# Kernel optimization log

Measured on AMD Instinct MI355X. Metric: run time of the kernel, lower is better.

Reference implementation:

```python
import jax, jax.numpy as jnp
import numpy as np

L = 8       # num decoder layers
S = 192     # seq_len = h*w = 24*8
D = 512     # d_model
DFF = 2048  # dim_feedforward
H, W, BS = 24, 8, 16
EPS = 1e-5


def setup_inputs() -> dict:
    key = jax.random.key(0)
    ks = jax.random.split(key, 8)
    f = jax.random.normal
    return {
        "q_feat": f(ks[0], (BS, D * L, H, W), jnp.float32),
        "g_feat": f(ks[1], (BS, D * L, H, W), jnp.float32),
        "targets": jax.random.randint(ks[2], (BS,), 0, 8),
        "score_embed": f(ks[3], (L, S, S), jnp.float32) * 0.05,
        "fc0_w": f(ks[4], (L, D, D), jnp.float32) * (1.0 / np.sqrt(D)),
        "fc0_b": jnp.zeros((L, D), jnp.float32),
        "bn1_g": jnp.ones((L,), jnp.float32),
        "bn1_b": jnp.zeros((L,), jnp.float32),
        "fc2_w": f(ks[5], (L, DFF, S), jnp.float32) * (1.0 / np.sqrt(S)),
        "fc2_b": jnp.zeros((L, DFF), jnp.float32),
        "bn2_g": jnp.ones((L, DFF), jnp.float32),
        "bn2_b": jnp.zeros((L, DFF), jnp.float32),
        "fc3_w": f(ks[6], (L, DFF), jnp.float32) * (1.0 / np.sqrt(DFF)),
        "fc3_b": jnp.zeros((L,), jnp.float32),
        "bn3_g": jnp.ones((L,), jnp.float32),
        "bn3_b": jnp.zeros((L,), jnp.float32),
    }


def _layer(qf, gf, se, w0, b0, g1, b1, w2, b2, g2, bb2, w3, b3, g3, bb3):
    # qf: [q,s,d], gf: [k,s,d]; shared fc0 projection for query and key
    query = jnp.einsum('qsd,ed->qse', qf, w0) + b0
    key_ = jnp.einsum('ksd,ed->kse', gf, w0) + b0
    # 4D correlation volume masked by sigmoid of learned score embedding
    score = jnp.einsum('qtd,ksd->qkst', query, key_) * jax.nn.sigmoid(se)
    q, k = score.shape[0], score.shape[1]
    sc = score.reshape(q * k, S, S)
    cat = jnp.concatenate([sc.max(axis=1), sc.max(axis=2)], axis=-1)  # [qk, 2S]
    x = cat.reshape(-1, S)  # [2qk, S]  (matches torch view(-1,1,S))
    # bn1: single channel -> normalize over all elements (training-mode BN)
    x = g1 * (x - x.mean()) * jax.lax.rsqrt(x.var() + EPS) + b1
    x = x @ w2.T + b2  # [2qk, DFF]
    mu = x.mean(0)
    var = x.var(0)
    x = g2 * (x - mu) * jax.lax.rsqrt(var + EPS) + bb2
    x = jax.nn.relu(x)
    x = x @ w3 + b3  # [2qk]
    x = x.reshape(-1, 2).sum(-1)  # [qk]: sum of row-max branch and col-max branch
    x = g3 * (x - x.mean()) * jax.lax.rsqrt(x.var() + EPS) + bb3
    return x.reshape(q, k)


def reference(q_feat, g_feat, targets, score_embed, fc0_w, fc0_b, bn1_g, bn1_b,
              fc2_w, fc2_b, bn2_g, bn2_b, fc3_w, fc3_b, bn3_g, bn3_b):
    bs = q_feat.shape[0]
    qf = jnp.transpose(q_feat, (0, 2, 3, 1)).reshape(bs, S, D * L)
    gf = jnp.transpose(g_feat, (0, 2, 3, 1)).reshape(bs, S, D * L)
    score = None
    for i in range(L):  # fixed small layer loop; each layer has distinct params
        si = _layer(qf[..., i * D:(i + 1) * D], gf[..., i * D:(i + 1) * D],
                    score_embed[i], fc0_w[i], fc0_b[i], bn1_g[i], bn1_b[i],
                    fc2_w[i], fc2_b[i], bn2_g[i], bn2_b[i],
                    fc3_w[i], fc3_b[i], bn3_g[i], bn3_b[i])
        score = si if score is None else score + si
    pair_labels = (targets[:, None] == targets[None, :]).astype(jnp.float32)
    return score, pair_labels
```

## Files before the change

kernel.cpp:

```cpp
#include <hip/hip_runtime.h>
#include <hip/hip_bf16.h>


#define EPS_ 1e-5f

typedef __attribute__((ext_vector_type(8))) _Float16 fp16x8;
typedef __attribute__((ext_vector_type(4)))  float   f32x4;
typedef __attribute__((ext_vector_type(16))) float   f32x16;

__device__ __forceinline__ unsigned fkey(float f) {
    unsigned u = __float_as_uint(f);
    return (u & 0x80000000u) ? ~u : (u | 0x80000000u);
}
__device__ __forceinline__ float funkey(unsigned k) {
    return (k & 0x80000000u) ? __uint_as_float(k & 0x7FFFFFFFu)
                             : __uint_as_float(~k);
}
__device__ __forceinline__ void gld16(const void* gp, void* lp) {
    __builtin_amdgcn_global_load_lds(
        (const __attribute__((address_space(1))) unsigned*)gp,
        (__attribute__((address_space(3))) unsigned*)lp, 16, 0, 0);
}

__global__ __launch_bounds__(256) void k_prep(const float* __restrict__ se,
                                              float* __restrict__ sig,
                                              const float* __restrict__ w2,
                                              _Float16* __restrict__ w2h,
                                              unsigned* __restrict__ xkey,
                                              float* __restrict__ bn2z,
                                              const float* __restrict__ w0,
                                              _Float16* __restrict__ w0h) {
    int b = blockIdx.x;
    int tid = threadIdx.x;
    if (b < 3072) {
        int i = b * 256 + tid;
        float4 v = *(const float4*)(w2 + (size_t)i * 4);
        _Float16 h[4] = {(_Float16)v.x, (_Float16)v.y, (_Float16)v.z, (_Float16)v.w};
        *(uint2*)(w2h + (size_t)i * 4) = *(uint2*)h;
    } else if (b < 3360) {
        int i = (b - 3072) * 256 + tid;
        float4 v = *(const float4*)(se + (size_t)i * 4);
        float4 o;
        o.x = 1.f / (1.f + __expf(-v.x));
        o.y = 1.f / (1.f + __expf(-v.y));
        o.z = 1.f / (1.f + __expf(-v.z));
        o.w = 1.f / (1.f + __expf(-v.w));
        *(float4*)(sig + (size_t)i * 4) = o;
    } else if (b < 3552) {
        int i = (b - 3360) * 256 + tid;
        uint4 z = {0u, 0u, 0u, 0u};
        uint4* p = (uint4*)xkey + (size_t)i * 4;
        p[0] = z; p[1] = z; p[2] = z; p[3] = z;
    } else if (b < 3585) {
        int i = (b - 3552) * 256 + tid;
        if (i < 8196) {
            float4 z = {0.f, 0.f, 0.f, 0.f};
            *(float4*)(bn2z + (size_t)i * 4) = z;
        }
    } else {
        int g = (b - 3585) * 256 + tid;
        int l  = g >> 15;
        int r  = g & 32767;
        int ks = r >> 12;
        int rr = r & 4095;
        int e  = rr >> 3;
        int ch = rr & 7;
        const float* src = w0 + (size_t)l * 262144 + (size_t)e * 512 + ks * 64 + ch * 8;
        float4 v0 = *(const float4*)src;
        float4 v1 = *(const float4*)(src + 4);
        fp16x8 h;
        h[0] = (_Float16)v0.x; h[1] = (_Float16)v0.y; h[2] = (_Float16)v0.z; h[3] = (_Float16)v0.w;
        h[4] = (_Float16)v1.x; h[5] = (_Float16)v1.y; h[6] = (_Float16)v1.z; h[7] = (_Float16)v1.w;
        size_t dst = ((size_t)(l * 8 + ks) * 512 + e) * 8 + (ch ^ (e & 7));
        *(fp16x8*)(w0h + dst * 8) = h;
    }
}

__global__ __launch_bounds__(512, 4) void k_fc0(const float* __restrict__ qfeat,
                                                const float* __restrict__ gfeat,
                                                const _Float16* __restrict__ w0h,
                                                const float* __restrict__ b0,
                                                _Float16* __restrict__ Qh) {
    int bid = blockIdx.x;
    int blo = bid & 7;
    int et  = (bid >> 3) & 3;
    int bhi = (bid >> 5) & 1;
    int sel = (bid >> 6) & 1;
    int l   = bid >> 7;
    int b   = blo + bhi * 8;

    const float* feat = sel ? gfeat : qfeat;
    const float* Af = feat + (size_t)b * 786432 + (size_t)l * 98304;

    __shared__ __align__(16) char smem[81920];

    int tid = threadIdx.x;
    int lane = tid & 63;
    int w = tid >> 6;
    int wm = w >> 2, wn = w & 3;
    int c = lane & 15;
    int hi4 = lane >> 4;

    int s0 = tid, s1 = tid + 512, s2 = tid + 1024;
    int ch0 = s0 / 192, t0 = s0 - ch0 * 192;
    int ch1 = s1 / 192, t1 = s1 - ch1 * 192;
    int ch2 = s2 / 192, t2 = s2 - ch2 * 192;
    const float* ap0 = Af + ch0 * 1536 + t0;
    const float* ap1 = Af + ch1 * 1536 + t1;
    const float* ap2 = Af + ch2 * 1536 + t2;
    int aw0 = t0 * 128 + ((ch0 ^ (t0 & 7)) << 4);
    int aw1 = t1 * 128 + ((ch1 ^ (t1 & 7)) << 4);
    int aw2 = t2 * 128 + ((ch2 ^ (t2 & 7)) << 4);

    f32x4 acc[6][2];
    #pragma unroll
    for (int mi = 0; mi < 6; mi++)
        #pragma unroll
        for (int nj = 0; nj < 2; nj++)
            #pragma unroll
            for (int r = 0; r < 4; r++) acc[mi][nj][r] = 0.f;

    float rA[3][8];

    auto ALOAD = [&](int ks) {
        int off = ks * 12288;
        #pragma unroll
        for (int j = 0; j < 8; j++) rA[0][j] = ap0[off + j * 192];
        #pragma unroll
        for (int j = 0; j < 8; j++) rA[1][j] = ap1[off + j * 192];
        #pragma unroll
        for (int j = 0; j < 8; j++) rA[2][j] = ap2[off + j * 192];
    };
    auto WLOAD = [&](int ks, int buf) {
        const _Float16* wp = w0h + ((size_t)(l * 8 + ks) * 512 + et * 128) * 64;
        char* d = smem + 49152 + buf * 16384;
        #pragma unroll
        for (int p = 0; p < 2; p++)
            gld16(wp + (size_t)(tid + p * 512) * 8, d + (tid + p * 512) * 16);
    };
    auto AWRITE = [&](int buf) {
        char* db = smem + buf * 24576;
        fp16x8 h0, h1, h2;
        #pragma unroll
        for (int j = 0; j < 8; j++) h0[j] = (_Float16)rA[0][j];
        #pragma unroll
        for (int j = 0; j < 8; j++) h1[j] = (_Float16)rA[1][j];
        #pragma unroll
        for (int j = 0; j < 8; j++) h2[j] = (_Float16)rA[2][j];
        *(fp16x8*)(db + aw0) = h0;
        *(fp16x8*)(db + aw1) = h1;
        *(fp16x8*)(db + aw2) = h2;
    };
    auto COMPUTE = [&](int buf) {
        const char* Ab = smem + buf * 24576;
        const char* Wb = smem + 49152 + buf * 16384;
        fp16x8 afr[6][2], bfr[2][2];
        #pragma unroll
        for (int mi = 0; mi < 6; mi++) {
            int tr = wm * 96 + mi * 16 + c;
            #pragma unroll
            for (int k2 = 0; k2 < 2; k2++) {
                int ph = (k2 * 4 + hi4) ^ (tr & 7);
                afr[mi][k2] = *(const fp16x8*)(Ab + tr * 128 + ph * 16);
            }
        }
        #pragma unroll
        for (int nj = 0; nj < 2; nj++) {
            int er = wn * 32 + nj * 16 + c;
            #pragma unroll
            for (int k2 = 0; k2 < 2; k2++) {
                int ph = (k2 * 4 + hi4) ^ (er & 7);
                bfr[nj][k2] = *(const fp16x8*)(Wb + er * 128 + ph * 16);
            }
        }
        #pragma unroll
        for (int k2 = 0; k2 < 2; k2++)
            #pragma unroll
            for (int mi = 0; mi < 6; mi++)
                #pragma unroll
                for (int nj = 0; nj < 2; nj++)
                    acc[mi][nj] = __builtin_amdgcn_mfma_f32_16x16x32_f16(
                        afr[mi][k2], bfr[nj][k2], acc[mi][nj], 0, 0, 0);
    };

    ALOAD(0); WLOAD(0, 0); AWRITE(0);
    __syncthreads();
    #pragma unroll
    for (int ks = 0; ks < 8; ks++) {
        int cur = ks & 1, nxt = cur ^ 1;
        if (ks < 7) { ALOAD(ks + 1); WLOAD(ks + 1, nxt); }
        COMPUTE(cur);
        if (ks < 7) AWRITE(nxt);
        __syncthreads();
    }

    __syncthreads();
    _Float16* lb = (_Float16*)smem;
    int rq = hi4 * 4;
    #pragma unroll
    for (int nj = 0; nj < 2; nj++) {
        int col = wn * 32 + nj * 16 + c;
        float bias = b0[l * 512 + et * 128 + col];
        #pragma unroll
        for (int mi = 0; mi < 6; mi++) {
            int tb = wm * 96 + mi * 16 + rq;
            #pragma unroll
            for (int r = 0; r < 4; r++)
                lb[(tb + r) * 128 + col] = (_Float16)(acc[mi][nj][r] + bias);
        }
    }
    __syncthreads();
    _Float16* Ob = Qh + ((size_t)(sel * 8 + l) * 16 + b) * 98304 + et * 128;
    #pragma unroll
    for (int p = 0; p < 6; p++) {
        int v = tid + p * 512;
        int t = v >> 4;
        int e = (v & 15) * 8;
        *(fp16x8*)(Ob + (size_t)t * 512 + e) = *(const fp16x8*)(lb + t * 128 + e);
    }
}

#define BARP() do { __builtin_amdgcn_s_barrier(); \
                    __builtin_amdgcn_sched_barrier(0); } while (0)

__global__ __launch_bounds__(512, 2) void k_score(const _Float16* __restrict__ Qh,
                                                  const float* __restrict__ sig,
                                                  unsigned* __restrict__ xkey,
                                                  int base) {
    int bid = blockIdx.x + base;
    int l = bid & 7;
    int tau = bid >> 3;
    int mt = tau % 12;
    int nt = tau / 12;
    int m0 = mt * 256, n0 = nt * 256;

    const char* Ag = (const char*)(Qh + (size_t)(8 + l) * 1572864);
    const char* Bg = (const char*)(Qh + (size_t)l * 1572864);

    __shared__ __align__(16) char smem[131072];

    int tid = threadIdx.x;
    int lane = tid & 63;
    int w = tid >> 6;
    int wm = w >> 2, wn = w & 3;
    int c = lane & 15;
    int hi4 = lane >> 4;

    int pk0 = ((hi4)     ^ (c & 7)) * 16;
    int pk1 = ((4 + hi4) ^ (c & 7)) * 16;
    char* aBase = smem + wm * 16384 + c * 128;
    char* bBase = smem + 65536 + (wn >> 1) * 16384 + ((wn & 1) * 64 + c) * 128;

    int rl = lane >> 3;
    int qsw = ((lane & 7) ^ rl) * 16;
    const char* Asrc = Ag + (size_t)(m0 + w * 8 + rl) * 1024 + qsw;
    const char* Bsrc = Bg + (size_t)(n0 + w * 8 + rl) * 1024 + qsw;
    char* aSt = smem + w * 1024;
    char* bSt = smem + 65536 + w * 1024;

    f32x4 acc[8][4];
    #pragma unroll
    for (int mi = 0; mi < 8; mi++)
        #pragma unroll
        for (int nj = 0; nj < 4; nj++)
            #pragma unroll
            for (int r = 0; r < 4; r++) acc[mi][nj][r] = 0.f;

    fp16x8 a[4][2], b01[2][2], b23[2][2];

    auto STA = [&](int t, int h) {
        if (t < 8) {
            const char* s = Asrc + (size_t)(h * 128) * 1024 + t * 128;
            char* d = aSt + (t & 1) * 32768 + h * 16384;
            gld16(s, d);
            gld16(s + 64 * 1024, d + 8192);
        }
    };
    auto STB = [&](int t, int h) {
        if (t < 8) {
            const char* s = Bsrc + (size_t)(h * 128) * 1024 + t * 128;
            char* d = bSt + (t & 1) * 32768 + h * 16384;
            gld16(s, d);
            gld16(s + 64 * 1024, d + 8192);
        }
    };
    auto LDA = [&](int t, int mh) {
        const char* p = aBase + (t & 1) * 32768 + mh * 8192;
        #pragma unroll
        for (int m = 0; m < 4; m++) {
            a[m][0] = *(const fp16x8*)(p + m * 2048 + pk0);
            a[m][1] = *(const fp16x8*)(p + m * 2048 + pk1);
        }
    };
    auto LDB = [&](int t, int nh, fp16x8 (&bb)[2][2]) {
        const char* p = bBase + (t & 1) * 32768 + nh * 4096;
        #pragma unroll
        for (int n = 0; n < 2; n++) {
            bb[n][0] = *(const fp16x8*)(p + n * 2048 + pk0);
            bb[n][1] = *(const fp16x8*)(p + n * 2048 + pk1);
        }
    };
    auto MM = [&](int mh, int nh, fp16x8 (&bb)[2][2]) {
        #pragma unroll
        for (int ks = 0; ks < 2; ks++)
            #pragma unroll
            for (int m = 0; m < 4; m++)
                #pragma unroll
                for (int n = 0; n < 2; n++)
                    acc[mh * 4 + m][nh * 2 + n] = __builtin_amdgcn_mfma_f32_16x16x32_f16(
                        a[m][ks], bb[n][ks], acc[mh * 4 + m][nh * 2 + n], 0, 0, 0);
    };

    STB(0, 0); STB(0, 1); STA(0, 0); STA(0, 1); STB(1, 0); STB(1, 1);
    asm volatile("s_waitcnt vmcnt(4)");
    BARP();

    #pragma unroll
    for (int it = 0; it < 4; it++) {
        int T = 2 * it, U = 2 * it + 1;
        LDA(T, 0); LDB(T, 0, b01); STA(U, 0); BARP();
        __builtin_amdgcn_s_setprio(1); MM(0, 0, b01); __builtin_amdgcn_s_setprio(0); BARP();
        LDB(T, 1, b23); STA(U, 1); BARP();
        __builtin_amdgcn_s_setprio(1); MM(0, 1, b23); __builtin_amdgcn_s_setprio(0); BARP();
        LDA(T, 1); STB(T + 2, 0); BARP();
        __builtin_amdgcn_s_setprio(1); MM(1, 0, b01); __builtin_amdgcn_s_setprio(0); BARP();
        STB(T + 2, 1); BARP();
        __builtin_amdgcn_s_setprio(1); MM(1, 1, b23); __builtin_amdgcn_s_setprio(0);
        if (it < 3) { asm volatile("s_waitcnt vmcnt(4)"); }
        else        { asm volatile("s_waitcnt vmcnt(0)"); }
        BARP();
        LDA(U, 0); LDB(U, 0, b01); STA(T + 2, 0); BARP();
        __builtin_amdgcn_s_setprio(1); MM(0, 0, b01); __builtin_amdgcn_s_setprio(0); BARP();
        LDB(U, 1, b23); STA(T + 2, 1); BARP();
        __builtin_amdgcn_s_setprio(1); MM(0, 1, b23); __builtin_amdgcn_s_setprio(0); BARP();
        LDA(U, 1); STB(T + 3, 0); BARP();
        __builtin_amdgcn_s_setprio(1); MM(1, 0, b01); __builtin_amdgcn_s_setprio(0); BARP();
        STB(T + 3, 1); BARP();
        __builtin_amdgcn_s_setprio(1); MM(1, 1, b23); __builtin_amdgcn_s_setprio(0);
        if (it < 3) { asm volatile("s_waitcnt vmcnt(4)"); }
        BARP();
    }

    __syncthreads();

    int rq = hi4 * 4;
    int gcb = n0 + wn * 64;
    int qq = gcb / 192;
    int tb = gcb - qq * 192;
    (void)qq;
    const float* sg = sig + (size_t)l * 36864;

    float rowm[8][4];
    float colm[2][4];
    #pragma unroll
    for (int mi = 0; mi < 8; mi++)
        #pragma unroll
        for (int r = 0; r < 4; r++) rowm[mi][r] = -3.4e38f;
    #pragma unroll
    for (int h = 0; h < 2; h++)
        #pragma unroll
        for (int nj = 0; nj < 4; nj++) colm[h][nj] = -3.4e38f;

    #pragma unroll
    for (int mi = 0; mi < 8; mi++) {
        int gm = m0 + wm * 128 + mi * 16;
        int sb = gm % 192;
        #pragma unroll
        for (int r = 0; r < 4; r++) {
            const float* sp = sg + (size_t)(sb + rq + r) * 192 + tb;
            #pragma unroll
            for (int nj = 0; nj < 4; nj++) {
                float v = acc[mi][nj][r] * sp[nj * 16 + c];
                rowm[mi][r] = fmaxf(rowm[mi][r], v);
                colm[mi >> 2][nj] = fmaxf(colm[mi >> 2][nj], v);
            }
        }
    }
    #pragma unroll
    for (int st = 1; st <= 8; st <<= 1)
        #pragma unroll
        for (int mi = 0; mi < 8; mi++)
            #pragma unroll
            for (int r = 0; r < 4; r++)
                rowm[mi][r] = fmaxf(rowm[mi][r], __shfl_xor(rowm[mi][r], st));
    #pragma unroll
    for (int h = 0; h < 2; h++)
        #pragma unroll
        for (int nj = 0; nj < 4; nj++) {
            colm[h][nj] = fmaxf(colm[h][nj], __shfl_xor(colm[h][nj], 16));
            colm[h][nj] = fmaxf(colm[h][nj], __shfl_xor(colm[h][nj], 32));
        }

    unsigned* red = (unsigned*)smem;
    if (c == 0) {
        #pragma unroll
        for (int mi = 0; mi < 8; mi++)
            #pragma unroll
            for (int r = 0; r < 4; r++)
                red[w * 256 + mi * 16 + rq + r] = fkey(rowm[mi][r]);
    }
    if (lane < 16) {
        #pragma unroll
        for (int h = 0; h < 2; h++)
            #pragma unroll
            for (int nj = 0; nj < 4; nj++)
                red[w * 256 + 128 + h * 64 + nj * 16 + lane] = fkey(colm[h][nj]);
    }
    __syncthreads();
    #pragma unroll
    for (int pass = 0; pass < 4; pass++) {
        int flat = pass * 512 + tid;
        unsigned val = red[flat];
        int ww = flat >> 8;
        int rem = flat & 255;
        int wmf = ww >> 2, wnf = ww & 3;
        int gcbf = n0 + wnf * 64;
        int qqf = gcbf / 192;
        size_t addr;
        if (rem < 128) {
            int gmf = m0 + wmf * 128 + rem;
            int kkf = gmf / 192;
            int sf = gmf - kkf * 192;
            addr = ((size_t)l * 512 + 2 * (qqf * 16 + kkf) + 1) * 192 + sf;
        } else {
            int ii = rem - 128;
            int hh = ii >> 6, cc = ii & 63;
            int kkf = (m0 + wmf * 128 + hh * 64) / 192;
            addr = ((size_t)l * 512 + 2 * (qqf * 16 + kkf)) * 192 + (gcbf - qqf * 192) + cc;
        }
        atomicMax(&xkey[addr], val);
    }
}

__global__ __launch_bounds__(256) void k_bn1s(const unsigned* __restrict__ xkey,
                                              float* __restrict__ bn1acc) {
    int l = blockIdx.x / 48;
    int b = blockIdx.x - l * 48;
    const unsigned* xk = xkey + (size_t)l * 98304 + b * 2048;
    int tid = threadIdx.x;
    uint4 v1 = *(const uint4*)(xk + tid * 8);
    uint4 v2 = *(const uint4*)(xk + tid * 8 + 4);
    float s = 0.f, s2 = 0.f;
    float e;
    e = funkey(v1.x); s += e; s2 += e * e;
    e = funkey(v1.y); s += e; s2 += e * e;
    e = funkey(v1.z); s += e; s2 += e * e;
    e = funkey(v1.w); s += e; s2 += e * e;
    e = funkey(v2.x); s += e; s2 += e * e;
    e = funkey(v2.y); s += e; s2 += e * e;
    e = funkey(v2.z); s += e; s2 += e * e;
    e = funkey(v2.w); s += e; s2 += e * e;
    #pragma unroll
    for (int o = 32; o; o >>= 1) { s += __shfl_down(s, o); s2 += __shfl_down(s2, o); }
    if ((tid & 63) == 0) {
        atomicAdd(&bn1acc[l * 2], s);
        atomicAdd(&bn1acc[l * 2 + 1], s2);
    }
}

__global__ __launch_bounds__(256) void k_bn1n(const unsigned* __restrict__ xkey,
                                              const float* __restrict__ bn1acc,
                                              const float* __restrict__ g1,
                                              const float* __restrict__ b1,
                                              _Float16* __restrict__ xh) {
    int idx = blockIdx.x * 256 + threadIdx.x;
    int l = idx / 24576;
    float mu = bn1acc[l * 2] * (1.f / 98304.f);
    float var = bn1acc[l * 2 + 1] * (1.f / 98304.f) - mu * mu;
    float a1 = g1[l] * rsqrtf(var + EPS_);
    float c1 = b1[l] - mu * a1;
    uint4 kv = *(const uint4*)(xkey + (size_t)idx * 4);
    _Float16 h[4];
    h[0] = (_Float16)(funkey(kv.x) * a1 + c1);
    h[1] = (_Float16)(funkey(kv.y) * a1 + c1);
    h[2] = (_Float16)(funkey(kv.z) * a1 + c1);
    h[3] = (_Float16)(funkey(kv.w) * a1 + c1);
    *(uint2*)(xh + (size_t)idx * 4) = *(uint2*)h;
}

__global__ __launch_bounds__(256) void k_fc2(const _Float16* __restrict__ xh,
                                             const _Float16* __restrict__ w2h,
                                             const float* __restrict__ b2,
                                             _Float16* __restrict__ hb,
                                             float* __restrict__ bn2sum,
                                             float* __restrict__ bn2sq) {
    int bid = blockIdx.x;
    int l = bid >> 6;
    int rem = bid & 63;
    int mt = rem & 3, nt = rem >> 2;
    int m0 = mt * 128, n0 = nt * 128;
    const char* Ag = (const char*)(xh + (size_t)l * 98304);
    const char* Bg = (const char*)(w2h + (size_t)l * 393216);

    __shared__ __align__(16) char As[8192];
    __shared__ __align__(16) char Bs[8192];

    int tid = threadIdx.x;
    int lane = tid & 63;
    int w = tid >> 6;
    int wm = w >> 1, wn = w & 1;

    f32x4 acc[4][4];
    #pragma unroll
    for (int mi = 0; mi < 4; mi++)
        #pragma unroll
        for (int nj = 0; nj < 4; nj++)
            #pragma unroll
            for (int r = 0; r < 4; r++) acc[mi][nj][r] = 0.f;

    int srow = lane >> 2;
    int sseg = ((lane & 3) ^ ((srow >> 1) & 3)) * 16;
    int c = lane & 15;
    int kqp = (((lane >> 4) ^ ((c >> 1) & 3))) * 16;

    for (int d0 = 0; d0 < 384; d0 += 64) {
        __syncthreads();
        #pragma unroll
        for (int j = 0; j < 2; j++) {
            int r = w * 32 + j * 16 + srow;
            gld16(Ag + (size_t)(m0 + r) * 384 + d0 + sseg, As + (w * 32 + j * 16) * 64);
            gld16(Bg + (size_t)(n0 + r) * 384 + d0 + sseg, Bs + (w * 32 + j * 16) * 64);
        }
        __syncthreads();
        fp16x8 a[4], b[4];
        #pragma unroll
        for (int mi = 0; mi < 4; mi++)
            a[mi] = *(const fp16x8*)(As + (wm * 64 + mi * 16 + c) * 64 + kqp);
        #pragma unroll
        for (int nj = 0; nj < 4; nj++)
            b[nj] = *(const fp16x8*)(Bs + (wn * 64 + nj * 16 + c) * 64 + kqp);
        #pragma unroll
        for (int mi = 0; mi < 4; mi++)
            #pragma unroll
            for (int nj = 0; nj < 4; nj++)
                acc[mi][nj] = __builtin_amdgcn_mfma_f32_16x16x32_f16(a[mi], b[nj], acc[mi][nj], 0, 0, 0);
    }

    int rq = (lane >> 4) * 4;
    _Float16* ho = hb + (size_t)l * 1048576;
    float colsum[4], colsq[4];
    #pragma unroll
    for (int nj = 0; nj < 4; nj++) { colsum[nj] = 0.f; colsq[nj] = 0.f; }
    #pragma unroll
    for (int nj = 0; nj < 4; nj++) {
        int gf = n0 + wn * 64 + nj * 16 + c;
        float bias = b2[l * 2048 + gf];
        #pragma unroll
        for (int mi = 0; mi < 4; mi++) {
            #pragma unroll
            for (int r = 0; r < 4; r++) {
                int gm = m0 + wm * 64 + mi * 16 + rq + r;
                float v = acc[mi][nj][r] + bias;
                ho[(size_t)gm * 2048 + gf] = (_Float16)v;
                colsum[nj] += v;
                colsq[nj] += v * v;
            }
        }
    }
    #pragma unroll
    for (int nj = 0; nj < 4; nj++) {
        colsum[nj] += __shfl_xor(colsum[nj], 16);
        colsum[nj] += __shfl_xor(colsum[nj], 32);
        colsq[nj]  += __shfl_xor(colsq[nj], 16);
        colsq[nj]  += __shfl_xor(colsq[nj], 32);
    }
    if (lane < 16) {
        #pragma unroll
        for (int nj = 0; nj < 4; nj++) {
            int gf = n0 + wn * 64 + nj * 16 + lane;
            atomicAdd(&bn2sum[l * 2048 + gf], colsum[nj]);
            atomicAdd(&bn2sq[l * 2048 + gf], colsq[nj]);
        }
    }
}

__global__ __launch_bounds__(256) void k_coef(const float* __restrict__ bn2sum,
                                              const float* __restrict__ bn2sq,
                                              const float* __restrict__ g2,
                                              const float* __restrict__ bb2,
                                              float* __restrict__ coef) {
    int i = blockIdx.x * 256 + threadIdx.x;
    float mu = bn2sum[i] * (1.f / 512.f);
    float var = bn2sq[i] * (1.f / 512.f) - mu * mu;
    float a2 = g2[i] * rsqrtf(var + EPS_);
    coef[i] = a2;
    coef[16384 + i] = bb2[i] - mu * a2;
}

__global__ __launch_bounds__(256) void k_fc3(const _Float16* __restrict__ hb,
                                             const float* __restrict__ coef,
                                             const float* __restrict__ w3,
                                             const float* __restrict__ b3,
                                             float* __restrict__ ybuf) {
    int n = blockIdx.x & 511;
    int l = blockIdx.x >> 9;
    const _Float16* h = hb + ((size_t)l * 512 + n) * 2048;
    int tid = threadIdx.x;
    int f0 = tid * 8;
    fp16x8 hv = *(const fp16x8*)(h + f0);
    const float* cA = coef + l * 2048 + f0;
    const float* cC = coef + 16384 + l * 2048 + f0;
    const float* w3p = w3 + l * 2048 + f0;
    float4 a0 = *(const float4*)(cA), a1 = *(const float4*)(cA + 4);
    float4 c0 = *(const float4*)(cC), c1 = *(const float4*)(cC + 4);
    float4 w0 = *(const float4*)(w3p), w1 = *(const float4*)(w3p + 4);
    float sum = 0.f;
    float va[8] = {a0.x, a0.y, a0.z, a0.w, a1.x, a1.y, a1.z, a1.w};
    float vc[8] = {c0.x, c0.y, c0.z, c0.w, c1.x, c1.y, c1.z, c1.w};
    float vw[8] = {w0.x, w0.y, w0.z, w0.w, w1.x, w1.y, w1.z, w1.w};
    #pragma unroll
    for (int j = 0; j < 8; j++) {
        float v = (float)hv[j] * va[j] + vc[j];
        v = fmaxf(v, 0.f);
        sum += v * vw[j];
    }
    __shared__ float red[4];
    int lane = tid & 63, w = tid >> 6;
    #pragma unroll
    for (int o = 32; o; o >>= 1) sum += __shfl_down(sum, o);
    if (lane == 0) red[w] = sum;
    __syncthreads();
    if (tid == 0) ybuf[l * 512 + n] = red[0] + red[1] + red[2] + red[3] + b3[l];
}

__global__ __launch_bounds__(256) void k_final(const float* __restrict__ ybuf,
                                               const float* __restrict__ g3,
                                               const float* __restrict__ bb3,
                                               const int* __restrict__ targets,
                                               float* __restrict__ out) {
    int tid = threadIdx.x;
    __shared__ float red[8];
    float scoreacc = 0.f;
    for (int l = 0; l < 8; l++) {
        float z = ybuf[l * 512 + 2 * tid] + ybuf[l * 512 + 2 * tid + 1];
        float s = z, s2 = z * z;
        int lane = tid & 63, w = tid >> 6;
        #pragma unroll
        for (int o = 32; o; o >>= 1) { s += __shfl_down(s, o); s2 += __shfl_down(s2, o); }
        if (lane == 0) { red[w] = s; red[4 + w] = s2; }
        __syncthreads();
        float S1 = red[0] + red[1] + red[2] + red[3];
        float S2 = red[4] + red[5] + red[6] + red[7];
        float mu = S1 * (1.f / 256.f);
        float var = S2 * (1.f / 256.f) - mu * mu;
        float rstd = rsqrtf(var + EPS_);
        scoreacc += g3[l] * (z - mu) * rstd + bb3[l];
        __syncthreads();
    }
    out[tid] = scoreacc;
    int i = tid >> 4, j = tid & 15;
    out[256 + tid] = (targets[i] == targets[j]) ? 1.f : 0.f;
}

extern "C" void kernel_launch(void* const* d_in, const int* in_sizes, int n_in,
                              void* d_out, int out_size, void* d_ws, size_t ws_size,
                              hipStream_t stream) {
    const float* q_feat = (const float*)d_in[0];
    const float* g_feat = (const float*)d_in[1];
    const int*   targets = (const int*)d_in[2];
    const float* se     = (const float*)d_in[3];
    const float* fc0_w  = (const float*)d_in[4];
    const float* fc0_b  = (const float*)d_in[5];
    const float* bn1_g  = (const float*)d_in[6];
    const float* bn1_b  = (const float*)d_in[7];
    const float* fc2_w  = (const float*)d_in[8];
    const float* fc2_b  = (const float*)d_in[9];
    const float* bn2_g  = (const float*)d_in[10];
    const float* bn2_b  = (const float*)d_in[11];
    const float* fc3_w  = (const float*)d_in[12];
    const float* fc3_b  = (const float*)d_in[13];
    const float* bn3_g  = (const float*)d_in[14];
    const float* bn3_b  = (const float*)d_in[15];

    float* ws = (float*)d_ws;
    _Float16* Qh   = (_Float16*)ws;
    float*    sig  = ws + 12582912;
    unsigned* xkey = (unsigned*)(ws + 12877824);
    _Float16* xh   = (_Float16*)(ws + 13664256);
    _Float16* w2h  = (_Float16*)(ws + 14057472);
    _Float16* hb   = (_Float16*)(ws + 15630336);
    _Float16* w0h  = (_Float16*)(ws + 15630336);
    float* bn2sum = ws + 19824640;
    float* bn2sq  = ws + 19841024;
    float* bn1acc = ws + 19857408;
    float* ybuf   = ws + 19857424;
    float* out  = (float*)d_out;

    k_prep<<<4609, 256, 0, stream>>>(se, sig, fc2_w, w2h, xkey, bn2sum, fc0_w, w0h);
    k_fc0<<<1024, 512, 0, stream>>>(q_feat, g_feat, w0h, fc0_b, Qh);
    k_score<<<256, 512, 0, stream>>>(Qh, sig, xkey, 0);
    k_score<<<256, 512, 0, stream>>>(Qh, sig, xkey, 256);
    k_score<<<256, 512, 0, stream>>>(Qh, sig, xkey, 512);
    k_score<<<256, 512, 0, stream>>>(Qh, sig, xkey, 768);
    k_score<<<128, 512, 0, stream>>>(Qh, sig, xkey, 1024);
    k_bn1s<<<384, 256, 0, stream>>>(xkey, bn1acc);
    k_bn1n<<<768, 256, 0, stream>>>(xkey, bn1acc, bn1_g, bn1_b, xh);
    k_fc2<<<512, 256, 0, stream>>>(xh, w2h, fc2_b, hb, bn2sum, bn2sq);
    k_coef<<<64, 256, 0, stream>>>(bn2sum, bn2sq, bn2_g, bn2_b, sig);
    k_fc3<<<4096, 256, 0, stream>>>(hb, sig, fc3_w, fc3_b, ybuf);
    k_final<<<1, 256, 0, stream>>>(ybuf, bn3_g, bn3_b, targets, out);
}
```

Baseline: 383.1 us.

## Deepen fc0 prefetch, merge score launches, restructure fc3 to wave-per-row

The fc0 kernel now keeps two register stages of A-tile loads in flight, using explicit vmcnt waits and raw barriers instead of full __syncthreads, so global latency overlaps more with MFMA work. The five k_score launches are merged into one launch of 1152 blocks to cut launch gaps and tail effects. k_fc3 assigns one wavefront per row, with each block handling eight rows, which removes the shared-memory reduction and shrinks the grid. The risks are the hand-tuned vmcnt counts, which must match the exact number of issued loads, and the extra register pressure from the doubled A buffer.

```diff
diff --git a/kernel.cpp b/kernel.cpp
--- a/kernel.cpp
+++ b/kernel.cpp
@@ -120,16 +120,16 @@
             #pragma unroll
             for (int r = 0; r < 4; r++) acc[mi][nj][r] = 0.f;
 
-    float rA[3][8];
-
-    auto ALOAD = [&](int ks) {
+    float rA[2][3][8];
+
+    auto ALOAD = [&](int ks, int ring) {
         int off = ks * 12288;
         #pragma unroll
-        for (int j = 0; j < 8; j++) rA[0][j] = ap0[off + j * 192];
-        #pragma unroll
-        for (int j = 0; j < 8; j++) rA[1][j] = ap1[off + j * 192];
-        #pragma unroll
-        for (int j = 0; j < 8; j++) rA[2][j] = ap2[off + j * 192];
+        for (int j = 0; j < 8; j++) rA[ring][0][j] = ap0[off + j * 192];
+        #pragma unroll
+        for (int j = 0; j < 8; j++) rA[ring][1][j] = ap1[off + j * 192];
+        #pragma unroll
+        for (int j = 0; j < 8; j++) rA[ring][2][j] = ap2[off + j * 192];
     };
     auto WLOAD = [&](int ks, int buf) {
         const _Float16* wp = w0h + ((size_t)(l * 8 + ks) * 512 + et * 128) * 64;
@@ -138,15 +138,15 @@
         for (int p = 0; p < 2; p++)
             gld16(wp + (size_t)(tid + p * 512) * 8, d + (tid + p * 512) * 16);
     };
-    auto AWRITE = [&](int buf) {
+    auto AWRITE = [&](int buf, int ring) {
         char* db = smem + buf * 24576;
         fp16x8 h0, h1, h2;
         #pragma unroll
-        for (int j = 0; j < 8; j++) h0[j] = (_Float16)rA[0][j];
-        #pragma unroll
-        for (int j = 0; j < 8; j++) h1[j] = (_Float16)rA[1][j];
-        #pragma unroll
-        for (int j = 0; j < 8; j++) h2[j] = (_Float16)rA[2][j];
+        for (int j = 0; j < 8; j++) h0[j] = (_Float16)rA[ring][0][j];
+        #pragma unroll
+        for (int j = 0; j < 8; j++) h1[j] = (_Float16)rA[ring][1][j];
+        #pragma unroll
+        for (int j = 0; j < 8; j++) h2[j] = (_Float16)rA[ring][2][j];
         *(fp16x8*)(db + aw0) = h0;
         *(fp16x8*)(db + aw1) = h1;
         *(fp16x8*)(db + aw2) = h2;
@@ -183,15 +183,33 @@
                         afr[mi][k2], bfr[nj][k2], acc[mi][nj], 0, 0, 0);
     };
 
-    ALOAD(0); WLOAD(0, 0); AWRITE(0);
-    __syncthreads();
+    WLOAD(0, 0);
+    __builtin_amdgcn_sched_barrier(0);
+    ALOAD(0, 0);
+    AWRITE(0, 0);
+    WLOAD(1, 1);
+    __builtin_amdgcn_sched_barrier(0);
+    ALOAD(1, 1);
+    __builtin_amdgcn_sched_barrier(0);
+    asm volatile("s_waitcnt vmcnt(26) lgkmcnt(0)");
+    __builtin_amdgcn_s_barrier();
+    __builtin_amdgcn_sched_barrier(0);
+
     #pragma unroll
     for (int ks = 0; ks < 8; ks++) {
         int cur = ks & 1, nxt = cur ^ 1;
-        if (ks < 7) { ALOAD(ks + 1); WLOAD(ks + 1, nxt); }
+        if (ks < 7) WLOAD(ks + 1, nxt);
+        __builtin_amdgcn_sched_barrier(0);
+        if (ks < 6) ALOAD(ks + 2, cur);
         COMPUTE(cur);
-        if (ks < 7) AWRITE(nxt);
-        __syncthreads();
+        if (ks < 7) AWRITE(nxt, nxt);
+        if (ks < 7) {
+            __builtin_amdgcn_sched_barrier(0);
+            if (ks < 6) { asm volatile("s_waitcnt vmcnt(24) lgkmcnt(0)"); }
+            else        { asm volatile("s_waitcnt vmcnt(0) lgkmcnt(0)"); }
+            __builtin_amdgcn_s_barrier();
+            __builtin_amdgcn_sched_barrier(0);
+        }
     }
 
     __syncthreads();
@@ -592,35 +610,39 @@
                                              const float* __restrict__ w3,
                                              const float* __restrict__ b3,
                                              float* __restrict__ ybuf) {
-    int n = blockIdx.x & 511;
-    int l = blockIdx.x >> 9;
-    const _Float16* h = hb + ((size_t)l * 512 + n) * 2048;
+    int grp = blockIdx.x & 63;
+    int l = blockIdx.x >> 6;
     int tid = threadIdx.x;
-    int f0 = tid * 8;
-    fp16x8 hv = *(const fp16x8*)(h + f0);
-    const float* cA = coef + l * 2048 + f0;
-    const float* cC = coef + 16384 + l * 2048 + f0;
-    const float* w3p = w3 + l * 2048 + f0;
-    float4 a0 = *(const float4*)(cA), a1 = *(const float4*)(cA + 4);
-    float4 c0 = *(const float4*)(cC), c1 = *(const float4*)(cC + 4);
-    float4 w0 = *(const float4*)(w3p), w1 = *(const float4*)(w3p + 4);
-    float sum = 0.f;
-    float va[8] = {a0.x, a0.y, a0.z, a0.w, a1.x, a1.y, a1.z, a1.w};
-    float vc[8] = {c0.x, c0.y, c0.z, c0.w, c1.x, c1.y, c1.z, c1.w};
-    float vw[8] = {w0.x, w0.y, w0.z, w0.w, w1.x, w1.y, w1.z, w1.w};
-    #pragma unroll
-    for (int j = 0; j < 8; j++) {
-        float v = (float)hv[j] * va[j] + vc[j];
-        v = fmaxf(v, 0.f);
-        sum += v * vw[j];
-    }
-    __shared__ float red[4];
-    int lane = tid & 63, w = tid >> 6;
-    #pragma unroll
-    for (int o = 32; o; o >>= 1) sum += __shfl_down(sum, o);
-    if (lane == 0) red[w] = sum;
-    __syncthreads();
-    if (tid == 0) ybuf[l * 512 + n] = red[0] + red[1] + red[2] + red[3] + b3[l];
+    int w = tid >> 6, lane = tid & 63;
+    const float* cA = coef + l * 2048;
+    const float* cC = coef + 16384 + l * 2048;
+    const float* w3p = w3 + l * 2048;
+    #pragma unroll
+    for (int rr = 0; rr < 2; rr++) {
+        int n = grp * 8 + w + rr * 4;
+        const _Float16* h = hb + ((size_t)l * 512 + n) * 2048;
+        float sum = 0.f;
+        #pragma unroll
+        for (int q = 0; q < 4; q++) {
+            int f = q * 512 + lane * 8;
+            fp16x8 hv = *(const fp16x8*)(h + f);
+            float4 a0 = *(const float4*)(cA + f), a1 = *(const float4*)(cA + f + 4);
+            float4 c0 = *(const float4*)(cC + f), c1 = *(const float4*)(cC + f + 4);
+            float4 w0 = *(const float4*)(w3p + f), w1 = *(const float4*)(w3p + f + 4);
+            float va[8] = {a0.x, a0.y, a0.z, a0.w, a1.x, a1.y, a1.z, a1.w};
+            float vc[8] = {c0.x, c0.y, c0.z, c0.w, c1.x, c1.y, c1.z, c1.w};
+            float vw[8] = {w0.x, w0.y, w0.z, w0.w, w1.x, w1.y, w1.z, w1.w};
+            #pragma unroll
+            for (int j = 0; j < 8; j++) {
+                float v = (float)hv[j] * va[j] + vc[j];
+                v = fmaxf(v, 0.f);
+                sum += v * vw[j];
+            }
+        }
+        #pragma unroll
+        for (int o = 32; o; o >>= 1) sum += __shfl_down(sum, o);
+        if (lane == 0) ybuf[l * 512 + n] = sum + b3[l];
+    }
 }
 
 __global__ __launch_bounds__(256) void k_final(const float* __restrict__ ybuf,
@@ -688,15 +710,11 @@
 
     k_prep<<<4609, 256, 0, stream>>>(se, sig, fc2_w, w2h, xkey, bn2sum, fc0_w, w0h);
     k_fc0<<<1024, 512, 0, stream>>>(q_feat, g_feat, w0h, fc0_b, Qh);
-    k_score<<<256, 512, 0, stream>>>(Qh, sig, xkey, 0);
-    k_score<<<256, 512, 0, stream>>>(Qh, sig, xkey, 256);
-    k_score<<<256, 512, 0, stream>>>(Qh, sig, xkey, 512);
-    k_score<<<256, 512, 0, stream>>>(Qh, sig, xkey, 768);
-    k_score<<<128, 512, 0, stream>>>(Qh, sig, xkey, 1024);
+    k_score<<<1152, 512, 0, stream>>>(Qh, sig, xkey, 0);
     k_bn1s<<<384, 256, 0, stream>>>(xkey, bn1acc);
     k_bn1n<<<768, 256, 0, stream>>>(xkey, bn1acc, bn1_g, bn1_b, xh);
     k_fc2<<<512, 256, 0, stream>>>(xh, w2h, fc2_b, hb, bn2sum, bn2sq);
     k_coef<<<64, 256, 0, stream>>>(bn2sum, bn2sq, bn2_g, bn2_b, sig);
-    k_fc3<<<4096, 256, 0, stream>>>(hb, sig, fc3_w, fc3_b, ybuf);
+    k_fc3<<<512, 256, 0, stream>>>(hb, sig, fc3_w, fc3_b, ybuf);
     k_final<<<1, 256, 0, stream>>>(ybuf, bn3_g, bn3_b, targets, out);
 }
```

Measured after the change: 431.4 us. +12.6%, slower.
